# Kernel tuning notes

Hardware: AMD Instinct MI355X
Metric: run time of the kernel (lower is better)

The kernel has to match this reference:

```python
import jax, jax.numpy as jnp
import numpy as np

B, S, D, H = 2, 2048, 768, 12
DEPTH = D // H


def setup_inputs() -> dict:
    key = jax.random.key(0)
    ks = jax.random.split(key, 8)
    scale = 1.0 / np.sqrt(D)
    inp = {
        "query": jax.random.normal(ks[0], (B, S, D), jnp.float32),
        "key": jax.random.normal(ks[1], (B, S, D), jnp.float32),
        "value": jax.random.normal(ks[2], (B, S, D), jnp.float32),
        # additive mask convention: 1.0 where attention is disallowed (causal)
        "mask": jnp.triu(jnp.ones((1, 1, S, S), jnp.float32), k=1),
        "Wq": jax.random.normal(ks[3], (D, D), jnp.float32) * scale,
        "bq": jnp.zeros((D,), jnp.float32),
        "Wk": jax.random.normal(ks[4], (D, D), jnp.float32) * scale,
        "bk": jnp.zeros((D,), jnp.float32),
        "Wv": jax.random.normal(ks[5], (D, D), jnp.float32) * scale,
        "bv": jnp.zeros((D,), jnp.float32),
        "Wo": jax.random.normal(ks[6], (D, D), jnp.float32) * scale,
        "bo": jnp.zeros((D,), jnp.float32),
    }
    return inp


def _split_heads(x):
    # [B, S, D] -> [B, H, S, depth]
    b, s, _ = x.shape
    return x.reshape(b, s, H, DEPTH).transpose(0, 2, 1, 3)


def reference(query, key, value, mask, Wq, bq, Wk, bk, Wv, bv, Wo, bo):
    q = _split_heads(query @ Wq + bq)   # [B,H,S,depth]
    k = _split_heads(key @ Wk + bk)
    v = _split_heads(value @ Wv + bv)

    d_k = jnp.asarray(DEPTH, q.dtype)
    logits = jnp.einsum("bhqd,bhkd->bhqk", q, k) / jnp.sqrt(d_k)
    logits = logits + mask * -1e9
    weights = jax.nn.softmax(logits, axis=-1)          # [B,H,S,S] -- O(N^2)
    attn = jnp.einsum("bhqk,bhkd->bhqd", weights, v)    # [B,H,S,depth]

    concat = attn.transpose(0, 2, 1, 3).reshape(query.shape[0], -1, D)
    return concat @ Wo + bo
```

## Files before the change

### kernel.cpp

```cpp
#include <hip/hip_runtime.h>


typedef __bf16 bf16;
typedef __bf16 bf16x8 __attribute__((ext_vector_type(8)));
typedef __bf16 bf16x4 __attribute__((ext_vector_type(4)));
typedef float  f32x4  __attribute__((ext_vector_type(4)));

__device__ __forceinline__ void async_load16(const void* g, void* l) {
  __builtin_amdgcn_global_load_lds(
      (__attribute__((address_space(1))) void*)g,
      (__attribute__((address_space(3))) void*)l, 16, 0, 0);
}

__global__ __launch_bounds__(256) void convert_kernel(
    const float* __restrict__ q, const float* __restrict__ k,
    const float* __restrict__ v, bf16* __restrict__ qo,
    bf16* __restrict__ ko, bf16* __restrict__ vo) {
  const float* src; bf16* dst;
  if (blockIdx.y == 0)      { src = q; dst = qo; }
  else if (blockIdx.y == 1) { src = k; dst = ko; }
  else                      { src = v; dst = vo; }
  size_t i = ((size_t)blockIdx.x * 256 + threadIdx.x) * 8;
  f32x4 a = *(const f32x4*)(src + i);
  f32x4 b = *(const f32x4*)(src + i + 4);
  bf16x8 o;
  o[0]=(bf16)a[0]; o[1]=(bf16)a[1]; o[2]=(bf16)a[2]; o[3]=(bf16)a[3];
  o[4]=(bf16)b[0]; o[5]=(bf16)b[1]; o[6]=(bf16)b[2]; o[7]=(bf16)b[3];
  *(bf16x8*)(dst + i) = o;
}

__global__ __launch_bounds__(256) void transpose_w_kernel(
    const float* __restrict__ W0, const float* __restrict__ W1,
    const float* __restrict__ W2, const float* __restrict__ W3,
    bf16* __restrict__ T0, bf16* __restrict__ T1,
    bf16* __restrict__ T2, bf16* __restrict__ T3) {
  const float* W; bf16* T;
  switch (blockIdx.z) {
    case 0: W = W0; T = T0; break;
    case 1: W = W1; T = T1; break;
    case 2: W = W2; T = T2; break;
    default: W = W3; T = T3; break;
  }
  __shared__ float tile[32][33];
  const int tx = threadIdx.x, ty = threadIdx.y;
  const int k0 = blockIdx.y * 32, n0 = blockIdx.x * 32;
#pragma unroll
  for (int j = 0; j < 32; j += 8)
    tile[ty + j][tx] = W[(size_t)(k0 + ty + j) * 768 + n0 + tx];
  __syncthreads();
#pragma unroll
  for (int j = 0; j < 32; j += 8) {
    int n = ty + j;
    T[(size_t)(n0 + n) * 768 + k0 + tx] = (bf16)tile[tx][n];
  }
}

__device__ __forceinline__ void gemm_body(
    const bf16* __restrict__ A, const bf16* __restrict__ Wt,
    const float* __restrict__ bias, void* __restrict__ outp,
    int m0, int n0, int mode, char* smem) {
  const int t = threadIdx.x;
  const int w = t >> 6, lane = t & 63;
  const int wm = w >> 1, wn = w & 1;
  const int quad = lane >> 4, l15 = lane & 15;
  const int srow = lane >> 3, k8p = lane & 7;

  size_t offA[4], offB[4];
  int ldsOff[4];
#pragma unroll
  for (int i = 0; i < 4; ++i) {
    const int rl = w * 32 + i * 8 + srow;
    const int kk = k8p ^ (rl & 7);
    offA[i] = (size_t)(m0 + rl) * 768 + kk * 8;
    offB[i] = (size_t)(n0 + rl) * 768 + kk * 8;
    ldsOff[i] = (w * 32 + i * 8) * 64;
  }

  f32x4 acc[4][4] = {};

#pragma unroll
  for (int i = 0; i < 4; ++i) {
    async_load16(A  + offA[i], smem + 2 * ldsOff[i]);
    async_load16(Wt + offB[i], smem + 16384 + 2 * ldsOff[i]);
  }

  for (int kidx = 0; kidx < 12; ++kidx) {
    __syncthreads();
    if (kidx < 11) {
      const int nb = (kidx + 1) & 1;
      const int k1 = (kidx + 1) * 64;
#pragma unroll
      for (int i = 0; i < 4; ++i) {
        async_load16(A  + offA[i] + k1, smem + nb * 32768 + 2 * ldsOff[i]);
        async_load16(Wt + offB[i] + k1, smem + nb * 32768 + 16384 + 2 * ldsOff[i]);
      }
    }
    const bf16* As = (const bf16*)(smem + (kidx & 1) * 32768);
    const bf16* Bs = (const bf16*)(smem + (kidx & 1) * 32768 + 16384);
#pragma unroll
    for (int ks = 0; ks < 2; ++ks) {
      bf16x8 af[4], bfv[4];
      const int slot = (((ks * 4 + quad) ^ (lane & 7)) * 8);
#pragma unroll
      for (int mi = 0; mi < 4; ++mi)
        af[mi] = *(const bf16x8*)(As + (wm * 64 + mi * 16 + l15) * 64 + slot);
#pragma unroll
      for (int ni = 0; ni < 4; ++ni)
        bfv[ni] = *(const bf16x8*)(Bs + (wn * 64 + ni * 16 + l15) * 64 + slot);
#pragma unroll
      for (int mi = 0; mi < 4; ++mi)
#pragma unroll
        for (int ni = 0; ni < 4; ++ni)
          acc[mi][ni] = __builtin_amdgcn_mfma_f32_16x16x32_bf16(af[mi], bfv[ni], acc[mi][ni], 0, 0, 0);
    }
  }

#pragma unroll
  for (int ni = 0; ni < 4; ++ni) {
    const float bc = bias[n0 + wn * 64 + ni * 16 + l15];
#pragma unroll
    for (int mi = 0; mi < 4; ++mi)
#pragma unroll
      for (int r = 0; r < 4; ++r) acc[mi][ni][r] += bc;
  }

  if (mode == 2) {
    float* outf = (float*)outp;
#pragma unroll
    for (int ni = 0; ni < 4; ++ni) {
      const int col = n0 + wn * 64 + ni * 16 + l15;
#pragma unroll
      for (int mi = 0; mi < 4; ++mi) {
        const int row = m0 + wm * 64 + mi * 16 + quad * 4;
#pragma unroll
        for (int r = 0; r < 4; ++r)
          outf[(size_t)(row + r) * 768 + col] = acc[mi][ni][r];
      }
    }
    return;
  }

  __syncthreads();
  bf16* outb = (bf16*)outp;
  if (mode == 0) {
    bf16* Ce = (bf16*)smem;
#pragma unroll
    for (int ni = 0; ni < 4; ++ni) {
      const int col = wn * 64 + ni * 16 + l15;
#pragma unroll
      for (int mi = 0; mi < 4; ++mi) {
        const int row = wm * 64 + mi * 16 + quad * 4;
#pragma unroll
        for (int r = 0; r < 4; ++r)
          Ce[(row + r) * 136 + col] = (bf16)acc[mi][ni][r];
      }
    }
    __syncthreads();
#pragma unroll
    for (int j = 0; j < 8; ++j) {
      const int ci = j * 256 + t;
      const int row = ci >> 4, c8 = (ci & 15) * 8;
      bf16x8 vv = *(const bf16x8*)(Ce + row * 136 + c8);
      const int rg = m0 + row, cg = n0 + c8;
      const int bb = rg >> 11, s = rg & 2047;
      const int h = cg >> 6, d = cg & 63;
      *(bf16x8*)(outb + ((size_t)(bb * 12 + h) * 2048 + s) * 64 + d) = vv;
    }
  } else {
    bf16* Ct = (bf16*)smem;
#pragma unroll
    for (int ni = 0; ni < 4; ++ni) {
      const int col = wn * 64 + ni * 16 + l15;
#pragma unroll
      for (int mi = 0; mi < 4; ++mi) {
        const int row = wm * 64 + mi * 16 + quad * 4;
        bf16x4 pv;
        pv[0] = (bf16)acc[mi][ni][0]; pv[1] = (bf16)acc[mi][ni][1];
        pv[2] = (bf16)acc[mi][ni][2]; pv[3] = (bf16)acc[mi][ni][3];
        *(bf16x4*)(Ct + (size_t)col * 136 + row) = pv;
      }
    }
    __syncthreads();
#pragma unroll
    for (int j = 0; j < 8; ++j) {
      const int ci = j * 256 + t;
      const int col = ci >> 4, r8 = (ci & 15) * 8;
      bf16x8 vv = *(const bf16x8*)(Ct + col * 136 + r8);
      const int cg = n0 + col;
      const int h = cg >> 6, d = cg & 63;
      const int rg = m0 + r8;
      const int bb = rg >> 11, s = rg & 2047;
      *(bf16x8*)(outb + ((size_t)(bb * 12 + h) * 64 + d) * 2048 + s) = vv;
    }
  }
}

__global__ __launch_bounds__(256) void gemm_qkv_kernel(
    const bf16* __restrict__ A0, const bf16* __restrict__ A1, const bf16* __restrict__ A2,
    const bf16* __restrict__ W0, const bf16* __restrict__ W1, const bf16* __restrict__ W2,
    const float* __restrict__ b0, const float* __restrict__ b1, const float* __restrict__ b2,
    bf16* __restrict__ Q, bf16* __restrict__ K, bf16* __restrict__ V) {
  __shared__ __align__(16) char smem[65536];
  const int z = blockIdx.z;
  const bf16* A  = (z == 0) ? A0 : (z == 1) ? A1 : A2;
  const bf16* Wt = (z == 0) ? W0 : (z == 1) ? W1 : W2;
  const float* bias = (z == 0) ? b0 : (z == 1) ? b1 : b2;
  void* outp = (z == 0) ? (void*)Q : (z == 1) ? (void*)K : (void*)V;
  gemm_body(A, Wt, bias, outp, blockIdx.y * 128, blockIdx.x * 128, (z == 2) ? 1 : 0, smem);
}

__global__ __launch_bounds__(256) void gemm_out_kernel(
    const bf16* __restrict__ A, const bf16* __restrict__ Wt,
    const float* __restrict__ bias, float* __restrict__ out) {
  __shared__ __align__(16) char smem[65536];
  gemm_body(A, Wt, bias, (void*)out, blockIdx.y * 128, blockIdx.x * 128, 2, smem);
}

__global__ __launch_bounds__(256) void attn_kernel(
    const bf16* __restrict__ Qh, const bf16* __restrict__ Kh,
    const bf16* __restrict__ Vt, float* __restrict__ O0, float* __restrict__ O1,
    float* __restrict__ L0, float* __restrict__ L1) {
  const int qt = 15 - (int)blockIdx.x;
  const int z = blockIdx.z;
  if (z == 1 && qt < 8) return;

  __shared__ __align__(16) char smem[49152];
  bf16* Ps = (bf16*)(smem + 32768);

  const int t = threadIdx.x;
  const int w = t >> 6, lane = t & 63, quad = lane >> 4, l15 = lane & 15;
  const int srow = lane >> 3, k8p = lane & 7;
  const int bh = blockIdx.y;
  const int q0 = qt * 128;
  const bf16* Qp = Qh + (size_t)bh * (2048 * 64);
  const bf16* Kp = Kh + (size_t)bh * (2048 * 64);
  const bf16* Vp = Vt + (size_t)bh * (64 * 2048);

  const int ntiles = 2 * qt + 2;
  const int kt_begin = z ? 16 : 0;
  const int kt_end = z ? ntiles : (ntiles < 16 ? ntiles : 16);

  size_t offK[2], offV[2];
  int ldsOff[2];
#pragma unroll
  for (int i = 0; i < 2; ++i) {
    const int rl = w * 16 + i * 8 + srow;
    const int kk = k8p ^ (rl & 7);
    offK[i] = (size_t)rl * 64 + kk * 8;
    offV[i] = (size_t)rl * 2048 + kk * 8;
    ldsOff[i] = (w * 16 + i * 8) * 64;
  }

  bf16x8 qf[2][2];
#pragma unroll
  for (int mi = 0; mi < 2; ++mi)
#pragma unroll
    for (int ks = 0; ks < 2; ++ks) {
      const int qrow = q0 + w * 32 + mi * 16 + l15;
      qf[mi][ks] = *(const bf16x8*)(Qp + (size_t)qrow * 64 + ks * 32 + quad * 8);
    }

  f32x4 o[2][4] = {};
  float lp[2] = {0.f, 0.f};

  const float sc = 0.125f * 1.44269504f;

#pragma unroll
  for (int i = 0; i < 2; ++i) {
    async_load16(Kp + offK[i] + (size_t)kt_begin * 64 * 64, smem + 2 * ldsOff[i]);
    async_load16(Vp + offV[i] + (size_t)kt_begin * 64,      smem + 8192 + 2 * ldsOff[i]);
  }

  for (int kt = kt_begin; kt < kt_end; ++kt) {
    const int k0 = kt * 64;
    const int cur = kt & 1;
    __syncthreads();
    if (kt + 1 < kt_end) {
      const int nb = cur ^ 1;
#pragma unroll
      for (int i = 0; i < 2; ++i) {
        async_load16(Kp + offK[i] + (size_t)(k0 + 64) * 64, smem + nb * 16384 + 2 * ldsOff[i]);
        async_load16(Vp + offV[i] + (k0 + 64),              smem + nb * 16384 + 8192 + 2 * ldsOff[i]);
      }
    }
    const bf16* Ks = (const bf16*)(smem + cur * 16384);
    const bf16* Vs = (const bf16*)(smem + cur * 16384 + 8192);

    f32x4 st[4][2] = {};
#pragma unroll
    for (int ks = 0; ks < 2; ++ks) {
      const int slot = (((ks * 4 + quad) ^ (lane & 7)) * 8);
      bf16x8 kf[4];
#pragma unroll
      for (int ni = 0; ni < 4; ++ni)
        kf[ni] = *(const bf16x8*)(Ks + (ni * 16 + l15) * 64 + slot);
#pragma unroll
      for (int ni = 0; ni < 4; ++ni)
#pragma unroll
        for (int mi = 0; mi < 2; ++mi)
          st[ni][mi] = __builtin_amdgcn_mfma_f32_16x16x32_bf16(kf[ni], qf[mi][ks], st[ni][mi], 0, 0, 0);
    }

    const bool diag = (k0 + 63 > q0);
#pragma unroll
    for (int mi = 0; mi < 2; ++mi) {
      const int q_local = w * 32 + mi * 16 + l15;
      const int qg = q0 + q_local;
#pragma unroll
      for (int ni = 0; ni < 4; ++ni) {
        bf16x4 pv;
#pragma unroll
        for (int r = 0; r < 4; ++r) {
          float p = __builtin_amdgcn_exp2f(st[ni][mi][r] * sc);
          if (diag && (k0 + ni * 16 + quad * 4 + r > qg)) p = 0.0f;
          lp[mi] += p;
          pv[r] = (bf16)p;
        }
        const int c = ni * 2 + (quad >> 1);
        *(bf16x4*)(Ps + q_local * 64 + ((c ^ (q_local & 7)) << 3) + ((quad & 1) << 2)) = pv;
      }
    }

#pragma unroll
    for (int ks = 0; ks < 2; ++ks) {
      const int slot = (((ks * 4 + quad) ^ (lane & 7)) * 8);
      bf16x8 pf[2], vfr[4];
#pragma unroll
      for (int mi = 0; mi < 2; ++mi)
        pf[mi] = *(const bf16x8*)(Ps + (w * 32 + mi * 16 + l15) * 64 + slot);
#pragma unroll
      for (int di = 0; di < 4; ++di)
        vfr[di] = *(const bf16x8*)(Vs + (di * 16 + l15) * 64 + slot);
#pragma unroll
      for (int mi = 0; mi < 2; ++mi)
#pragma unroll
        for (int di = 0; di < 4; ++di)
          o[mi][di] = __builtin_amdgcn_mfma_f32_16x16x32_bf16(pf[mi], vfr[di], o[mi][di], 0, 0, 0);
    }
  }

  float* Op; float* Lp_;
  size_t rbase;
  if (z == 0) { Op = O0; Lp_ = L0; rbase = (size_t)bh * 2048 + q0; }
  else        { Op = O1; Lp_ = L1; rbase = (size_t)bh * 1024 + (qt - 8) * 128; }

#pragma unroll
  for (int mi = 0; mi < 2; ++mi) {
    float l = lp[mi];
    l += __shfl_xor(l, 16);
    l += __shfl_xor(l, 32);
    if (quad == 0) Lp_[rbase + w * 32 + mi * 16 + l15] = l;
#pragma unroll
    for (int di = 0; di < 4; ++di) {
      const int d = di * 16 + l15;
#pragma unroll
      for (int r = 0; r < 4; ++r) {
        const size_t row = rbase + w * 32 + mi * 16 + quad * 4 + r;
        Op[row * 64 + d] = o[mi][di][r];
      }
    }
  }
}

__global__ __launch_bounds__(256) void combine_kernel(
    const float* __restrict__ O0, const float* __restrict__ O1,
    const float* __restrict__ L0, const float* __restrict__ L1,
    bf16* __restrict__ attb) {
  const int idx = blockIdx.x * 256 + threadIdx.x;
  const int row = idx >> 4;
  const int dd = (idx & 15) << 2;
  const int bh = row >> 11, s = row & 2047;
  f32x4 o = *(const f32x4*)(O0 + (size_t)row * 64 + dd);
  float l = L0[row];
  if (s >= 1024) {
    const size_t r1 = (size_t)bh * 1024 + (s - 1024);
    f32x4 o1 = *(const f32x4*)(O1 + r1 * 64 + dd);
    o[0] += o1[0]; o[1] += o1[1]; o[2] += o1[2]; o[3] += o1[3];
    l += L1[r1];
  }
  const float inv = 1.0f / l;
  bf16x4 ov;
  ov[0] = (bf16)(o[0] * inv); ov[1] = (bf16)(o[1] * inv);
  ov[2] = (bf16)(o[2] * inv); ov[3] = (bf16)(o[3] * inv);
  const int b = bh / 12, h = bh % 12;
  *(bf16x4*)(attb + ((size_t)(b * 2048 + s)) * 768 + h * 64 + dd) = ov;
}

extern "C" void kernel_launch(void* const* d_in, const int* in_sizes, int n_in,
                              void* d_out, int out_size, void* d_ws, size_t ws_size,
                              hipStream_t stream) {
  const float* query = (const float*)d_in[0];
  const float* key   = (const float*)d_in[1];
  const float* value = (const float*)d_in[2];
  const float* Wq = (const float*)d_in[4];
  const float* bq = (const float*)d_in[5];
  const float* Wk = (const float*)d_in[6];
  const float* bk = (const float*)d_in[7];
  const float* Wv = (const float*)d_in[8];
  const float* bv = (const float*)d_in[9];
  const float* Wo = (const float*)d_in[10];
  const float* bo = (const float*)d_in[11];
  float* out = (float*)d_out;

  char* ws = (char*)d_ws;
  constexpr size_t SZ_X = (size_t)4096 * 768 * 2;
  constexpr size_t SZ_W = (size_t)768 * 768 * 2;
  bf16* qb   = (bf16*)(ws);
  bf16* kb   = (bf16*)(ws + SZ_X);
  bf16* vb   = (bf16*)(ws + 2 * SZ_X);
  bf16* wtq  = (bf16*)(ws + 3 * SZ_X);
  bf16* wtk  = (bf16*)(ws + 3 * SZ_X + SZ_W);
  bf16* wtv  = (bf16*)(ws + 3 * SZ_X + 2 * SZ_W);
  bf16* wto  = (bf16*)(ws + 3 * SZ_X + 3 * SZ_W);
  bf16* Qh   = (bf16*)(ws + 3 * SZ_X + 4 * SZ_W);
  bf16* Kh   = (bf16*)(ws + 4 * SZ_X + 4 * SZ_W);
  bf16* Vtb  = (bf16*)(ws + 5 * SZ_X + 4 * SZ_W);
  bf16* attb = (bf16*)(ws + 6 * SZ_X + 4 * SZ_W);
  float* O0 = (float*)(ws);
  float* O1 = (float*)(ws + 2 * SZ_X);
  float* L0 = (float*)(ws + 3 * SZ_X);
  float* L1 = (float*)(ws + 3 * SZ_X + 196608);

  convert_kernel<<<dim3(1536, 3), 256, 0, stream>>>(query, key, value, qb, kb, vb);
  transpose_w_kernel<<<dim3(24, 24, 4), dim3(32, 8), 0, stream>>>(Wq, Wk, Wv, Wo, wtq, wtk, wtv, wto);
  gemm_qkv_kernel<<<dim3(6, 32, 3), 256, 0, stream>>>(qb, kb, vb, wtq, wtk, wtv, bq, bk, bv, Qh, Kh, Vtb);
  attn_kernel<<<dim3(16, 24, 2), 256, 0, stream>>>(Qh, Kh, Vtb, O0, O1, L0, L1);
  combine_kernel<<<dim3(3072), 256, 0, stream>>>(O0, O1, L0, L1, attb);
  gemm_out_kernel<<<dim3(6, 32), 256, 0, stream>>>(attb, wto, bo, out);
}
```

Measured before the change: 204.9 us.

## Fuse input conversion into QKV GEMM and split attention into four KV chunks

The separate fp32-to-bf16 conversion kernel is removed. The QKV GEMM now loads fp32 inputs into registers, converts them, and writes bf16 into swizzled LDS while the previous tile computes. Attention work is split into up to four 8-tile KV chunks per query tile, scheduled from a constant table (longest chunks first) over a flat 960-block grid. Partial outputs are stored in bf16 rather than fp32, and the combine kernel sums up to four partials. This removes a launch and a round trip of the inputs through memory, and balances the causal attention load across blocks. In exchange it adds register pressure in the GEMM, some bf16 rounding of partial sums, and more combine traffic.

```diff
diff --git a/kernel.cpp b/kernel.cpp
--- a/kernel.cpp
+++ b/kernel.cpp
@@ -12,22 +12,15 @@
       (__attribute__((address_space(3))) void*)l, 16, 0, 0);
 }
 
-__global__ __launch_bounds__(256) void convert_kernel(
-    const float* __restrict__ q, const float* __restrict__ k,
-    const float* __restrict__ v, bf16* __restrict__ qo,
-    bf16* __restrict__ ko, bf16* __restrict__ vo) {
-  const float* src; bf16* dst;
-  if (blockIdx.y == 0)      { src = q; dst = qo; }
-  else if (blockIdx.y == 1) { src = k; dst = ko; }
-  else                      { src = v; dst = vo; }
-  size_t i = ((size_t)blockIdx.x * 256 + threadIdx.x) * 8;
-  f32x4 a = *(const f32x4*)(src + i);
-  f32x4 b = *(const f32x4*)(src + i + 4);
-  bf16x8 o;
-  o[0]=(bf16)a[0]; o[1]=(bf16)a[1]; o[2]=(bf16)a[2]; o[3]=(bf16)a[3];
-  o[4]=(bf16)b[0]; o[5]=(bf16)b[1]; o[6]=(bf16)b[2]; o[7]=(bf16)b[3];
-  *(bf16x8*)(dst + i) = o;
-}
+__constant__ unsigned char chunk_tab[40] = {
+  3, 4, 5, 6, 7, 8, 9, 10, 11, 12, 13, 14, 15,
+  7 | 16, 8 | 16, 9 | 16, 10 | 16, 11 | 16, 12 | 16, 13 | 16, 14 | 16, 15 | 16,
+  11 | 32, 12 | 32, 13 | 32, 14 | 32, 15 | 32,
+  15 | 48,
+  2, 6 | 16, 10 | 32, 14 | 48,
+  1, 5 | 16, 9 | 32, 13 | 48,
+  0, 4 | 16, 8 | 32, 12 | 48,
+};
 
 __global__ __launch_bounds__(256) void transpose_w_kernel(
     const float* __restrict__ W0, const float* __restrict__ W1,
@@ -55,48 +48,83 @@
   }
 }
 
-__device__ __forceinline__ void gemm_body(
-    const bf16* __restrict__ A, const bf16* __restrict__ Wt,
-    const float* __restrict__ bias, void* __restrict__ outp,
-    int m0, int n0, int mode, char* smem) {
+__global__ __launch_bounds__(256) void gemm_qkv_kernel(
+    const float* __restrict__ X0, const float* __restrict__ X1, const float* __restrict__ X2,
+    const bf16* __restrict__ W0, const bf16* __restrict__ W1, const bf16* __restrict__ W2,
+    const float* __restrict__ b0, const float* __restrict__ b1, const float* __restrict__ b2,
+    bf16* __restrict__ Q, bf16* __restrict__ K, bf16* __restrict__ V) {
+  __shared__ __align__(16) char smem[65536];
+  const int z = blockIdx.z;
+  const float* A   = (z == 0) ? X0 : (z == 1) ? X1 : X2;
+  const bf16* Wt   = (z == 0) ? W0 : (z == 1) ? W1 : W2;
+  const float* bias = (z == 0) ? b0 : (z == 1) ? b1 : b2;
+  bf16* outb = (z == 0) ? Q : (z == 1) ? K : V;
+  const int mode = (z == 2) ? 1 : 0;
+  const int m0 = blockIdx.y * 128, n0 = blockIdx.x * 128;
+
   const int t = threadIdx.x;
   const int w = t >> 6, lane = t & 63;
   const int wm = w >> 1, wn = w & 1;
   const int quad = lane >> 4, l15 = lane & 15;
   const int srow = lane >> 3, k8p = lane & 7;
 
-  size_t offA[4], offB[4];
-  int ldsOff[4];
+  size_t offB[4]; int ldsOffB[4];
 #pragma unroll
   for (int i = 0; i < 4; ++i) {
     const int rl = w * 32 + i * 8 + srow;
     const int kk = k8p ^ (rl & 7);
-    offA[i] = (size_t)(m0 + rl) * 768 + kk * 8;
     offB[i] = (size_t)(n0 + rl) * 768 + kk * 8;
-    ldsOff[i] = (w * 32 + i * 8) * 64;
+    ldsOffB[i] = (w * 32 + i * 8) * 64;
+  }
+  const int arow0 = t >> 3;
+  const int ac = t & 7;
+  size_t offA[4]; int apos[4];
+#pragma unroll
+  for (int i = 0; i < 4; ++i) {
+    const int row = arow0 + i * 32;
+    offA[i] = (size_t)(m0 + row) * 768 + ac * 8;
+    apos[i] = row * 64 + ((ac ^ (row & 7)) << 3);
   }
 
   f32x4 acc[4][4] = {};
+  f32x4 pa[4], pb[4];
 
 #pragma unroll
   for (int i = 0; i < 4; ++i) {
-    async_load16(A  + offA[i], smem + 2 * ldsOff[i]);
-    async_load16(Wt + offB[i], smem + 16384 + 2 * ldsOff[i]);
+    pa[i] = *(const f32x4*)(A + offA[i]);
+    pb[i] = *(const f32x4*)(A + offA[i] + 4);
+  }
+#pragma unroll
+  for (int i = 0; i < 4; ++i)
+    async_load16(Wt + offB[i], smem + 16384 + 2 * ldsOffB[i]);
+  {
+    bf16* As0 = (bf16*)smem;
+#pragma unroll
+    for (int i = 0; i < 4; ++i) {
+      bf16x8 o;
+      o[0]=(bf16)pa[i][0]; o[1]=(bf16)pa[i][1]; o[2]=(bf16)pa[i][2]; o[3]=(bf16)pa[i][3];
+      o[4]=(bf16)pb[i][0]; o[5]=(bf16)pb[i][1]; o[6]=(bf16)pb[i][2]; o[7]=(bf16)pb[i][3];
+      *(bf16x8*)(As0 + apos[i]) = o;
+    }
   }
 
   for (int kidx = 0; kidx < 12; ++kidx) {
     __syncthreads();
+    const int cur = (kidx & 1) * 32768;
+    const int nb = ((kidx + 1) & 1) * 32768;
     if (kidx < 11) {
-      const int nb = (kidx + 1) & 1;
       const int k1 = (kidx + 1) * 64;
 #pragma unroll
       for (int i = 0; i < 4; ++i) {
-        async_load16(A  + offA[i] + k1, smem + nb * 32768 + 2 * ldsOff[i]);
-        async_load16(Wt + offB[i] + k1, smem + nb * 32768 + 16384 + 2 * ldsOff[i]);
-      }
-    }
-    const bf16* As = (const bf16*)(smem + (kidx & 1) * 32768);
-    const bf16* Bs = (const bf16*)(smem + (kidx & 1) * 32768 + 16384);
+        pa[i] = *(const f32x4*)(A + offA[i] + k1);
+        pb[i] = *(const f32x4*)(A + offA[i] + k1 + 4);
+      }
+#pragma unroll
+      for (int i = 0; i < 4; ++i)
+        async_load16(Wt + offB[i] + k1, smem + nb + 16384 + 2 * ldsOffB[i]);
+    }
+    const bf16* As = (const bf16*)(smem + cur);
+    const bf16* Bs = (const bf16*)(smem + cur + 16384);
 #pragma unroll
     for (int ks = 0; ks < 2; ++ks) {
       bf16x8 af[4], bfv[4];
@@ -113,6 +141,16 @@
         for (int ni = 0; ni < 4; ++ni)
           acc[mi][ni] = __builtin_amdgcn_mfma_f32_16x16x32_bf16(af[mi], bfv[ni], acc[mi][ni], 0, 0, 0);
     }
+    if (kidx < 11) {
+      bf16* Asn = (bf16*)(smem + nb);
+#pragma unroll
+      for (int i = 0; i < 4; ++i) {
+        bf16x8 o;
+        o[0]=(bf16)pa[i][0]; o[1]=(bf16)pa[i][1]; o[2]=(bf16)pa[i][2]; o[3]=(bf16)pa[i][3];
+        o[4]=(bf16)pb[i][0]; o[5]=(bf16)pb[i][1]; o[6]=(bf16)pb[i][2]; o[7]=(bf16)pb[i][3];
+        *(bf16x8*)(Asn + apos[i]) = o;
+      }
+    }
   }
 
 #pragma unroll
@@ -124,24 +162,7 @@
       for (int r = 0; r < 4; ++r) acc[mi][ni][r] += bc;
   }
 
-  if (mode == 2) {
-    float* outf = (float*)outp;
-#pragma unroll
-    for (int ni = 0; ni < 4; ++ni) {
-      const int col = n0 + wn * 64 + ni * 16 + l15;
-#pragma unroll
-      for (int mi = 0; mi < 4; ++mi) {
-        const int row = m0 + wm * 64 + mi * 16 + quad * 4;
-#pragma unroll
-        for (int r = 0; r < 4; ++r)
-          outf[(size_t)(row + r) * 768 + col] = acc[mi][ni][r];
-      }
-    }
-    return;
-  }
-
   __syncthreads();
-  bf16* outb = (bf16*)outp;
   if (mode == 0) {
     bf16* Ce = (bf16*)smem;
 #pragma unroll
@@ -195,34 +216,102 @@
   }
 }
 
-__global__ __launch_bounds__(256) void gemm_qkv_kernel(
-    const bf16* __restrict__ A0, const bf16* __restrict__ A1, const bf16* __restrict__ A2,
-    const bf16* __restrict__ W0, const bf16* __restrict__ W1, const bf16* __restrict__ W2,
-    const float* __restrict__ b0, const float* __restrict__ b1, const float* __restrict__ b2,
-    bf16* __restrict__ Q, bf16* __restrict__ K, bf16* __restrict__ V) {
-  __shared__ __align__(16) char smem[65536];
-  const int z = blockIdx.z;
-  const bf16* A  = (z == 0) ? A0 : (z == 1) ? A1 : A2;
-  const bf16* Wt = (z == 0) ? W0 : (z == 1) ? W1 : W2;
-  const float* bias = (z == 0) ? b0 : (z == 1) ? b1 : b2;
-  void* outp = (z == 0) ? (void*)Q : (z == 1) ? (void*)K : (void*)V;
-  gemm_body(A, Wt, bias, outp, blockIdx.y * 128, blockIdx.x * 128, (z == 2) ? 1 : 0, smem);
-}
-
 __global__ __launch_bounds__(256) void gemm_out_kernel(
     const bf16* __restrict__ A, const bf16* __restrict__ Wt,
     const float* __restrict__ bias, float* __restrict__ out) {
   __shared__ __align__(16) char smem[65536];
-  gemm_body(A, Wt, bias, (void*)out, blockIdx.y * 128, blockIdx.x * 128, 2, smem);
+  const int m0 = blockIdx.y * 128, n0 = blockIdx.x * 128;
+  const int t = threadIdx.x;
+  const int w = t >> 6, lane = t & 63;
+  const int wm = w >> 1, wn = w & 1;
+  const int quad = lane >> 4, l15 = lane & 15;
+  const int srow = lane >> 3, k8p = lane & 7;
+
+  size_t offA[4], offB[4];
+  int ldsOff[4];
+#pragma unroll
+  for (int i = 0; i < 4; ++i) {
+    const int rl = w * 32 + i * 8 + srow;
+    const int kk = k8p ^ (rl & 7);
+    offA[i] = (size_t)(m0 + rl) * 768 + kk * 8;
+    offB[i] = (size_t)(n0 + rl) * 768 + kk * 8;
+    ldsOff[i] = (w * 32 + i * 8) * 64;
+  }
+
+  f32x4 acc[4][4] = {};
+#pragma unroll
+  for (int i = 0; i < 4; ++i) {
+    async_load16(A  + offA[i], smem + 2 * ldsOff[i]);
+    async_load16(Wt + offB[i], smem + 16384 + 2 * ldsOff[i]);
+  }
+
+  for (int kidx = 0; kidx < 12; ++kidx) {
+    __syncthreads();
+    if (kidx < 11) {
+      const int nb = (kidx + 1) & 1;
+      const int k1 = (kidx + 1) * 64;
+#pragma unroll
+      for (int i = 0; i < 4; ++i) {
+        async_load16(A  + offA[i] + k1, smem + nb * 32768 + 2 * ldsOff[i]);
+        async_load16(Wt + offB[i] + k1, smem + nb * 32768 + 16384 + 2 * ldsOff[i]);
+      }
+    }
+    const bf16* As = (const bf16*)(smem + (kidx & 1) * 32768);
+    const bf16* Bs = (const bf16*)(smem + (kidx & 1) * 32768 + 16384);
+#pragma unroll
+    for (int ks = 0; ks < 2; ++ks) {
+      bf16x8 af[4], bfv[4];
+      const int slot = (((ks * 4 + quad) ^ (lane & 7)) * 8);
+#pragma unroll
+      for (int mi = 0; mi < 4; ++mi)
+        af[mi] = *(const bf16x8*)(As + (wm * 64 + mi * 16 + l15) * 64 + slot);
+#pragma unroll
+      for (int ni = 0; ni < 4; ++ni)
+        bfv[ni] = *(const bf16x8*)(Bs + (wn * 64 + ni * 16 + l15) * 64 + slot);
+#pragma unroll
+      for (int mi = 0; mi < 4; ++mi)
+#pragma unroll
+        for (int ni = 0; ni < 4; ++ni)
+          acc[mi][ni] = __builtin_amdgcn_mfma_f32_16x16x32_bf16(af[mi], bfv[ni], acc[mi][ni], 0, 0, 0);
+    }
+  }
+
+#pragma unroll
+  for (int ni = 0; ni < 4; ++ni) {
+    const float bc = bias[n0 + wn * 64 + ni * 16 + l15];
+#pragma unroll
+    for (int mi = 0; mi < 4; ++mi)
+#pragma unroll
+      for (int r = 0; r < 4; ++r) acc[mi][ni][r] += bc;
+  }
+
+#pragma unroll
+  for (int ni = 0; ni < 4; ++ni) {
+    const int col = n0 + wn * 64 + ni * 16 + l15;
+#pragma unroll
+    for (int mi = 0; mi < 4; ++mi) {
+      const int row = m0 + wm * 64 + mi * 16 + quad * 4;
+#pragma unroll
+      for (int r = 0; r < 4; ++r)
+        out[(size_t)(row + r) * 768 + col] = acc[mi][ni][r];
+    }
+  }
 }
 
 __global__ __launch_bounds__(256) void attn_kernel(
     const bf16* __restrict__ Qh, const bf16* __restrict__ Kh,
-    const bf16* __restrict__ Vt, float* __restrict__ O0, float* __restrict__ O1,
-    float* __restrict__ L0, float* __restrict__ L1) {
-  const int qt = 15 - (int)blockIdx.x;
-  const int z = blockIdx.z;
-  if (z == 1 && qt < 8) return;
+    const bf16* __restrict__ Vt,
+    bf16* __restrict__ O0, bf16* __restrict__ O1,
+    bf16* __restrict__ O2, bf16* __restrict__ O3,
+    float* __restrict__ L0, float* __restrict__ L1,
+    float* __restrict__ L2, float* __restrict__ L3) {
+  const int ent = chunk_tab[blockIdx.x / 24];
+  const int bh = blockIdx.x % 24;
+  const int qt = ent & 15, c = ent >> 4;
+  const int q0 = qt * 128;
+  const int kt_begin = c * 8;
+  const int ntiles = 2 * qt + 2;
+  const int kt_end = (kt_begin + 8 < ntiles) ? kt_begin + 8 : ntiles;
 
   __shared__ __align__(16) char smem[49152];
   bf16* Ps = (bf16*)(smem + 32768);
@@ -230,15 +319,9 @@
   const int t = threadIdx.x;
   const int w = t >> 6, lane = t & 63, quad = lane >> 4, l15 = lane & 15;
   const int srow = lane >> 3, k8p = lane & 7;
-  const int bh = blockIdx.y;
-  const int q0 = qt * 128;
   const bf16* Qp = Qh + (size_t)bh * (2048 * 64);
   const bf16* Kp = Kh + (size_t)bh * (2048 * 64);
   const bf16* Vp = Vt + (size_t)bh * (64 * 2048);
-
-  const int ntiles = 2 * qt + 2;
-  const int kt_begin = z ? 16 : 0;
-  const int kt_end = z ? ntiles : (ntiles < 16 ? ntiles : 16);
 
   size_t offK[2], offV[2];
   int ldsOff[2];
@@ -316,8 +399,8 @@
           lp[mi] += p;
           pv[r] = (bf16)p;
         }
-        const int c = ni * 2 + (quad >> 1);
-        *(bf16x4*)(Ps + q_local * 64 + ((c ^ (q_local & 7)) << 3) + ((quad & 1) << 2)) = pv;
+        const int cc = ni * 2 + (quad >> 1);
+        *(bf16x4*)(Ps + q_local * 64 + ((cc ^ (q_local & 7)) << 3) + ((quad & 1) << 2)) = pv;
       }
     }
 
@@ -339,10 +422,15 @@
     }
   }
 
-  float* Op; float* Lp_;
-  size_t rbase;
-  if (z == 0) { Op = O0; Lp_ = L0; rbase = (size_t)bh * 2048 + q0; }
-  else        { Op = O1; Lp_ = L1; rbase = (size_t)bh * 1024 + (qt - 8) * 128; }
+  bf16* Op; float* Lp_;
+  switch (c) {
+    case 0: Op = O0; Lp_ = L0; break;
+    case 1: Op = O1; Lp_ = L1; break;
+    case 2: Op = O2; Lp_ = L2; break;
+    default: Op = O3; Lp_ = L3; break;
+  }
+  const int rows_c = 2048 - 512 * c;
+  const size_t rbase = (size_t)bh * rows_c + (q0 - 512 * c);
 
 #pragma unroll
   for (int mi = 0; mi < 2; ++mi) {
@@ -356,32 +444,50 @@
 #pragma unroll
       for (int r = 0; r < 4; ++r) {
         const size_t row = rbase + w * 32 + mi * 16 + quad * 4 + r;
-        Op[row * 64 + d] = o[mi][di][r];
+        Op[row * 64 + d] = (bf16)o[mi][di][r];
       }
     }
   }
 }
 
 __global__ __launch_bounds__(256) void combine_kernel(
-    const float* __restrict__ O0, const float* __restrict__ O1,
+    const bf16* __restrict__ O0, const bf16* __restrict__ O1,
+    const bf16* __restrict__ O2, const bf16* __restrict__ O3,
     const float* __restrict__ L0, const float* __restrict__ L1,
+    const float* __restrict__ L2, const float* __restrict__ L3,
     bf16* __restrict__ attb) {
   const int idx = blockIdx.x * 256 + threadIdx.x;
   const int row = idx >> 4;
   const int dd = (idx & 15) << 2;
   const int bh = row >> 11, s = row & 2047;
-  f32x4 o = *(const f32x4*)(O0 + (size_t)row * 64 + dd);
+  float o0, o1, o2, o3;
+  {
+    bf16x4 v = *(const bf16x4*)(O0 + (size_t)row * 64 + dd);
+    o0 = (float)v[0]; o1 = (float)v[1]; o2 = (float)v[2]; o3 = (float)v[3];
+  }
   float l = L0[row];
+  if (s >= 512) {
+    const size_t r1 = (size_t)bh * 1536 + (s - 512);
+    bf16x4 v = *(const bf16x4*)(O1 + r1 * 64 + dd);
+    o0 += (float)v[0]; o1 += (float)v[1]; o2 += (float)v[2]; o3 += (float)v[3];
+    l += L1[r1];
+  }
   if (s >= 1024) {
-    const size_t r1 = (size_t)bh * 1024 + (s - 1024);
-    f32x4 o1 = *(const f32x4*)(O1 + r1 * 64 + dd);
-    o[0] += o1[0]; o[1] += o1[1]; o[2] += o1[2]; o[3] += o1[3];
-    l += L1[r1];
+    const size_t r2 = (size_t)bh * 1024 + (s - 1024);
+    bf16x4 v = *(const bf16x4*)(O2 + r2 * 64 + dd);
+    o0 += (float)v[0]; o1 += (float)v[1]; o2 += (float)v[2]; o3 += (float)v[3];
+    l += L2[r2];
+  }
+  if (s >= 1536) {
+    const size_t r3 = (size_t)bh * 512 + (s - 1536);
+    bf16x4 v = *(const bf16x4*)(O3 + r3 * 64 + dd);
+    o0 += (float)v[0]; o1 += (float)v[1]; o2 += (float)v[2]; o3 += (float)v[3];
+    l += L3[r3];
   }
   const float inv = 1.0f / l;
   bf16x4 ov;
-  ov[0] = (bf16)(o[0] * inv); ov[1] = (bf16)(o[1] * inv);
-  ov[2] = (bf16)(o[2] * inv); ov[3] = (bf16)(o[3] * inv);
+  ov[0] = (bf16)(o0 * inv); ov[1] = (bf16)(o1 * inv);
+  ov[2] = (bf16)(o2 * inv); ov[3] = (bf16)(o3 * inv);
   const int b = bh / 12, h = bh % 12;
   *(bf16x4*)(attb + ((size_t)(b * 2048 + s)) * 768 + h * 64 + dd) = ov;
 }
@@ -403,28 +509,26 @@
   float* out = (float*)d_out;
 
   char* ws = (char*)d_ws;
-  constexpr size_t SZ_X = (size_t)4096 * 768 * 2;
-  constexpr size_t SZ_W = (size_t)768 * 768 * 2;
-  bf16* qb   = (bf16*)(ws);
-  bf16* kb   = (bf16*)(ws + SZ_X);
-  bf16* vb   = (bf16*)(ws + 2 * SZ_X);
-  bf16* wtq  = (bf16*)(ws + 3 * SZ_X);
-  bf16* wtk  = (bf16*)(ws + 3 * SZ_X + SZ_W);
-  bf16* wtv  = (bf16*)(ws + 3 * SZ_X + 2 * SZ_W);
-  bf16* wto  = (bf16*)(ws + 3 * SZ_X + 3 * SZ_W);
-  bf16* Qh   = (bf16*)(ws + 3 * SZ_X + 4 * SZ_W);
-  bf16* Kh   = (bf16*)(ws + 4 * SZ_X + 4 * SZ_W);
-  bf16* Vtb  = (bf16*)(ws + 5 * SZ_X + 4 * SZ_W);
-  bf16* attb = (bf16*)(ws + 6 * SZ_X + 4 * SZ_W);
-  float* O0 = (float*)(ws);
-  float* O1 = (float*)(ws + 2 * SZ_X);
-  float* L0 = (float*)(ws + 3 * SZ_X);
-  float* L1 = (float*)(ws + 3 * SZ_X + 196608);
-
-  convert_kernel<<<dim3(1536, 3), 256, 0, stream>>>(query, key, value, qb, kb, vb);
+  bf16* wtq  = (bf16*)(ws);
+  bf16* wtk  = (bf16*)(ws + 1179648);
+  bf16* wtv  = (bf16*)(ws + 2359296);
+  bf16* wto  = (bf16*)(ws + 3538944);
+  bf16* Qh   = (bf16*)(ws + 4718592);
+  bf16* Kh   = (bf16*)(ws + 11010048);
+  bf16* Vtb  = (bf16*)(ws + 17301504);
+  bf16* attb = (bf16*)(ws + 23592960);
+  bf16* O0   = (bf16*)(ws + 29884416);
+  bf16* O1   = (bf16*)(ws + 36175872);
+  bf16* O2   = (bf16*)(ws + 40894464);
+  bf16* O3   = (bf16*)(ws + 44040192);
+  float* L0  = (float*)(ws + 45613056);
+  float* L1  = (float*)(ws + 45809664);
+  float* L2  = (float*)(ws + 45957120);
+  float* L3  = (float*)(ws + 46055424);
+
   transpose_w_kernel<<<dim3(24, 24, 4), dim3(32, 8), 0, stream>>>(Wq, Wk, Wv, Wo, wtq, wtk, wtv, wto);
-  gemm_qkv_kernel<<<dim3(6, 32, 3), 256, 0, stream>>>(qb, kb, vb, wtq, wtk, wtv, bq, bk, bv, Qh, Kh, Vtb);
-  attn_kernel<<<dim3(16, 24, 2), 256, 0, stream>>>(Qh, Kh, Vtb, O0, O1, L0, L1);
-  combine_kernel<<<dim3(3072), 256, 0, stream>>>(O0, O1, L0, L1, attb);
+  gemm_qkv_kernel<<<dim3(6, 32, 3), 256, 0, stream>>>(query, key, value, wtq, wtk, wtv, bq, bk, bv, Qh, Kh, Vtb);
+  attn_kernel<<<dim3(960), 256, 0, stream>>>(Qh, Kh, Vtb, O0, O1, O2, O3, L0, L1, L2, L3);
+  combine_kernel<<<dim3(3072), 256, 0, stream>>>(O0, O1, O2, O3, L0, L1, L2, L3, attb);
   gemm_out_kernel<<<dim3(6, 32), 256, 0, stream>>>(attb, wto, bo, out);
 }
```

Measured after the change: 203.9 us. No clear change (-0.5%).
